# Kernel tuning notes

Hardware: AMD Instinct MI355X
Metric: run time of the kernel (lower is better)

Reference implementation:

```python
import jax, jax.numpy as jnp
import numpy as np
from math import comb

N_DERIV = 4          # num_derivatives
ODE_DIM = 512        # ode_dimension
K = ODE_DIM * (N_DERIV + 1)


def _build_system(n, d):
    # system_matrices_1d: A_1d = flip(pascal), Q_1d = flip(hilbert), chol(Q_1d)
    x = np.arange(n + 1)
    B = np.array([[comb(i, j) for j in range(n + 1)] for i in range(n + 1)], dtype=np.float64)
    A1 = B[::-1, ::-1]                                  # flip both axes
    Hil = 1.0 / (x[:, None] + x[None, :] + 1.0)
    Q1 = Hil[::-1, ::-1]
    L1 = np.linalg.cholesky(Q1)
    a = np.kron(np.eye(d), A1)
    q = np.kron(np.eye(d), L1)
    return jnp.asarray(a, jnp.float32), jnp.asarray(q, jnp.float32)


def _qr_r(x):
    # sqrtm_to_cholesky: upper-triangular factor from reduced QR
    return jnp.linalg.qr(x)[1]


def setup_inputs() -> dict:
    key = jax.random.key(0)
    k1, k2, k3, k4, k5 = jax.random.split(key, 5)
    a, q_sqrtm_lower = _build_system(N_DERIV, ODE_DIM)
    m0 = jax.random.normal(k1, (K,), dtype=jnp.float32)
    l0 = jnp.tril(jax.random.normal(k2, (K, K), dtype=jnp.float32) * 0.05)
    H = jax.random.normal(k3, (ODE_DIM, K), dtype=jnp.float32) * 0.1
    bias = jax.random.normal(k4, (ODE_DIM,), dtype=jnp.float32)
    dt = jax.random.uniform(k5, (1,), dtype=jnp.float32, minval=0.05, maxval=0.15)
    return {"m0": m0, "l0": l0, "H": H, "bias": bias, "dt": dt,
            "a": a, "q_sqrtm_lower": q_sqrtm_lower}


def reference(m0, l0, H, bias, dt, a, q_sqrtm_lower):
    d = H.shape[0]
    k = m0.shape[0]
    n1 = k // d                       # num_derivatives + 1
    # --- assemble_preconditioner ---
    powers = jnp.arange(n1 - 1, -1, -1, dtype=m0.dtype)
    scales = jnp.exp(jax.lax.lgamma(powers + 1.0))
    pw = powers + 0.5
    adt = jnp.abs(dt[0])
    p = jnp.tile(adt ** pw / scales, d)          # (k,)
    p_inv = jnp.tile(adt ** (-pw) * scales, d)   # (k,)
    # --- extrapolate_mean ---
    m0_p = p_inv * m0
    m_ext_p = a @ m0_p
    m_ext = p * m_ext_p
    # EK-style linearized observation residual
    m_obs = H @ m_ext - bias                     # (d,)
    # --- estimate_error ---
    l_obs_ns_e = H @ (p_inv[:, None] * q_sqrtm_lower)            # (d,k)
    l_obs_raw = _qr_r(l_obs_ns_e.T).T                            # lower (d,d)
    res_white = jax.scipy.linalg.solve_triangular(l_obs_raw.T, m_obs, lower=False)
    diffusion = jnp.sqrt(jnp.dot(res_white, res_white) / res_white.size)
    error = diffusion * jnp.sqrt(jnp.einsum('nj,nj->n', l_obs_raw, l_obs_raw))
    # --- complete_extrapolation (sum_of_sqrtm_factors) ---
    R1 = (a @ (p_inv[:, None] * l0)).T           # (k,k)
    R2 = (diffusion * q_sqrtm_lower).T           # (k,k)
    l_ext_p = _qr_r(jnp.vstack([R1, R2])).T      # lower (k,k)
    l_ext = p[:, None] * l_ext_p
    # --- final_correction ---
    l_obs_ns = H @ l_ext                         # (d,k)
    l_obs = _qr_r(l_obs_ns.T).T                  # lower (d,d)
    crosscov = l_ext @ l_obs_ns.T                # (k,d)
    gain = jax.scipy.linalg.cho_solve((l_obs, True), crosscov.T).T  # (k,d)
    m_cor = m_ext - gain @ m_obs
    l_cor = l_ext - gain @ l_obs_ns
    u = jnp.reshape(m_cor, (-1, d), order='F')[0]  # derivative-0 block
    return m_cor, l_cor, u, error, diffusion
```

## Files before the change

kernel.cpp:

```cpp
#include <hip/hip_runtime.h>
#include <math.h>

#define KDIM 2560
#define DDIM 512
#define NB 64

#define QM 2560
#define QM2 1024
#define QN 512
#define PW 16
#define QACT 528

#define OUT_LCOR 2560
#define OUT_U    6556160
#define OUT_ERR  6556672
#define OUT_DIFF 6557184


__global__ void k_setup(const float* dt, double* scal){
  if (threadIdx.x==0 && blockIdx.x==0){
    double adt = fabs((double)dt[0]);
    const double scales[5] = {24.0,6.0,2.0,1.0,1.0};
    for (int i=0;i<5;i++){
      double pw = (double)(4-i)+0.5;
      scal[i]   = pow(adt, pw)/scales[i];
      scal[5+i] = pow(adt,-pw)*scales[i];
    }
  }
}

__global__ __launch_bounds__(256) void k_mext_mobs(const float* a, const float* m0, const float* H,
                                                   const float* bias, const double* scal,
                                                   double* mext, double* mobs){
  __shared__ double me[KDIM];
  __shared__ double red[256];
  double pp[5], pv[5];
  #pragma unroll
  for (int i=0;i<5;i++){ pp[i]=scal[i]; pv[i]=scal[5+i]; }
  int tid=threadIdx.x;
  for (int r=tid; r<KDIM; r+=256){
    int j=r/5, i=r%5;
    const float* arow = a + (size_t)r*KDIM + 5*j;
    const float* m0b  = m0 + 5*j;
    double acc=0;
    #pragma unroll
    for (int l=0;l<5;l++) acc += (double)arow[l]*pv[l]*(double)m0b[l];
    me[r] = pp[i]*acc;
  }
  __syncthreads();
  if (blockIdx.x==0) for (int r=tid;r<KDIM;r+=256) mext[r]=me[r];
  int b = blockIdx.x;
  const float* Hr = H + (size_t)b*KDIM;
  double acc=0;
  for (int c=tid;c<KDIM;c+=256) acc += (double)Hr[c]*me[c];
  red[tid]=acc; __syncthreads();
  for (int s=128;s>0;s>>=1){ if (tid<s) red[tid]+=red[tid+s]; __syncthreads(); }
  if (tid==0) mobs[b] = red[0] - (double)bias[b];
}

__global__ void k_A2(const float* H, const float* q, const double* scal,
                     double* Atop, double* Abot){
  int idx = blockIdx.x*blockDim.x+threadIdx.x;
  if (idx >= QN*QM) return;
  double pv[5];
  #pragma unroll
  for (int t=0;t<5;t++) pv[t]=scal[5+t];
  int j = idx / QM;
  int i = idx % QM;
  int bi = i/5;
  double acc=0;
  #pragma unroll
  for (int t=0;t<5;t++)
    acc += (double)H[(size_t)j*QM + 5*bi+t]*pv[t]*(double)q[(size_t)(5*bi+t)*QM + i];
  if (i < 512) Atop[(size_t)j*QM2 + i] = acc;
  else         Abot[(size_t)j*2048 + (i-512)] = acc;
}

__global__ void k_copyB(const double* Gbot, double* AQ){
  int idx = blockIdx.x*blockDim.x+threadIdx.x;
  if (idx >= 512*512) return;
  int c = idx/512, rr = idx%512;
  AQ[(size_t)c*QM2 + 512 + rr] = (rr<=c) ? Gbot[(size_t)c*512 + rr] : 0.0;
}

__global__ __launch_bounds__(576) void qr_step(double* A, double* vhead, double* Tbufs, int p){
  int col0 = p*PW;
  int tid=threadIdx.x, wid=tid>>6, lane=tid&63;

  if (blockIdx.x > 0){
    int pc0 = col0 - PW;
    const double* T = Tbufs + (size_t)(p-1)*PW*PW;
    int cc = col0 + PW + ((int)blockIdx.x - 1);
    int m = QM2 - pc0; if (m>QACT) m=QACT;
    __shared__ double redu[9][PW];
    __shared__ double yshu[PW];
    __shared__ double wshu[PW];
    int lr = tid;
    double a = (lr<m)? A[(size_t)cc*QM2 + pc0 + lr] : 0.0;
    double vv[PW];
    #pragma unroll
    for (int j=0;j<PW;j++){
      double vj=0.0;
      if (lr<m){
        if (lr>j)       vj=A[(size_t)(pc0+j)*QM2 + pc0 + lr];
        else if (lr==j) vj=vhead[pc0+j];
      }
      vv[j]=vj;
    }
    #pragma unroll
    for (int j=0;j<PW;j++){
      double d=vv[j]*a;
      #pragma unroll
      for (int o=32;o>0;o>>=1) d+=__shfl_down(d,o);
      if (lane==0) redu[wid][j]=d;
    }
    __syncthreads();
    if (tid<PW){
      double y=0;
      #pragma unroll
      for (int t=0;t<9;t++) y+=redu[t][tid];
      yshu[tid]=y;
    }
    __syncthreads();
    if (tid<PW){
      double s=0;
      for (int t=0;t<=tid;t++) s+=T[t*PW+tid]*yshu[t];
      wshu[tid]=s;
    }
    __syncthreads();
    if (lr<m){
      double s=0;
      #pragma unroll
      for (int j=0;j<PW;j++) s+=vv[j]*wshu[j];
      A[(size_t)cc*QM2 + pc0 + lr]=a-s;
    }
    return;
  }

  __shared__ double redw[9][PW];
  __shared__ double rednorm[9];
  __shared__ double sh[3];
  __shared__ double wsh[PW];
  __shared__ double alphas[PW], betas[PW];
  __shared__ double VtVs[PW][PW];
  __shared__ double Tsh[PW][PW];
  __shared__ double redP[9][PW*PW];
  __shared__ double ysh2[PW][PW];
  __shared__ double wsh2[PW][PW];

  int m = QM2 - col0; if (m>QACT) m=QACT;
  bool on = tid < m;
  double x[PW];

  if (p>0){
    int pc0 = col0 - PW;
    const double* T = Tbufs + (size_t)(p-1)*PW*PW;
    int mp = QM2 - pc0; if (mp>QACT) mp=QACT;
    bool gA = on;
    bool gB = (tid>=560);
    int rowA = col0 + tid;
    int kB   = tid - 560;
    double vv[PW];
    #pragma unroll
    for (int j=0;j<PW;j++){
      double vj=0.0;
      if (gA){
        if (tid + PW < mp) vj = A[(size_t)(pc0+j)*QM2 + rowA];
      } else if (gB){
        if (kB>j)       vj=A[(size_t)(pc0+j)*QM2 + pc0 + kB];
        else if (kB==j) vj=vhead[pc0+j];
      }
      vv[j]=vj;
    }
    #pragma unroll
    for (int c=0;c<PW;c++){
      double a=0.0;
      if (gA)      a = A[(size_t)(col0+c)*QM2 + rowA];
      else if (gB) a = A[(size_t)(col0+c)*QM2 + pc0 + kB];
      x[c]=a;
    }
    #pragma unroll
    for (int c=0;c<PW;c++){
      #pragma unroll
      for (int j=0;j<PW;j++){
        double d=vv[j]*x[c];
        #pragma unroll
        for (int o=32;o>0;o>>=1) d+=__shfl_down(d,o);
        if (lane==0) redP[wid][c*PW+j]=d;
      }
    }
    __syncthreads();
    if (tid<PW*PW){
      double y=0;
      #pragma unroll
      for (int t=0;t<9;t++) y+=redP[t][tid];
      ysh2[tid>>4][tid&15]=y;
    }
    __syncthreads();
    if (tid<PW*PW){
      int c=tid>>4, jj=tid&15;
      double s=0;
      for (int t=0;t<=jj;t++) s+=T[t*PW+jj]*ysh2[c][t];
      wsh2[c][jj]=s;
    }
    __syncthreads();
    #pragma unroll
    for (int c=0;c<PW;c++){
      double s=0;
      #pragma unroll
      for (int j=0;j<PW;j++) s+=vv[j]*wsh2[c][j];
      x[c]-=s;
    }
    if (gB){
      #pragma unroll
      for (int c=0;c<PW;c++) A[(size_t)(col0+c)*QM2 + pc0 + kB] = x[c];
    }
    if (!on){
      #pragma unroll
      for (int c=0;c<PW;c++) x[c]=0.0;
    }
    __syncthreads();
  } else {
    #pragma unroll
    for (int j=0;j<PW;j++)
      x[j] = on ? A[(size_t)(col0+j)*QM2 + col0 + tid] : 0.0;
  }

  #pragma unroll
  for (int j=0;j<PW;j++){
    double v0 = (tid>=j && on)? x[j] : 0.0;
    double ps = v0*v0;
    #pragma unroll
    for (int o=32;o>0;o>>=1) ps += __shfl_down(ps,o);
    if (lane==0) rednorm[wid]=ps;
    if (tid==j) sh[0]=x[j];
    __syncthreads();
    if (tid==0){
      double s0=0;
      for (int t=0;t<9;t++) s0+=rednorm[t];
      double x1=sh[0];
      double nrm=sqrt(s0);
      double alpha=(x1>=0.0)?-nrm:nrm;
      double v1=x1-alpha;
      double vtv=s0-2.0*alpha*x1+alpha*alpha;
      double b=(vtv>0.0)?2.0/vtv:0.0;
      sh[1]=v1; sh[2]=b;
      alphas[j]=alpha; betas[j]=b;
      vhead[col0+j]=v1;
    }
    __syncthreads();
    if (tid==j) x[j]=sh[1];
    double b=sh[2];
    double v=(tid>=j && on)? x[j] : 0.0;
    #pragma unroll
    for (int t=0;t<PW;t++){
      if (t==j) continue;
      double pdot=v*x[t];
      #pragma unroll
      for (int o=32;o>0;o>>=1) pdot+=__shfl_down(pdot,o);
      if (lane==0) redw[wid][t]=pdot;
    }
    __syncthreads();
    if (tid<PW && tid!=j){
      double tot=0;
      #pragma unroll
      for (int t2=0;t2<9;t2++) tot+=redw[t2][tid];
      if (tid>j) wsh[tid]=b*tot;
      else       VtVs[tid][j]=tot;
    }
    __syncthreads();
    if (v!=0.0){
      #pragma unroll
      for (int t=j+1;t<PW;t++) x[t]-=wsh[t]*v;
    }
  }
  __syncthreads();
  if (tid<PW){
    int i=tid;
    Tsh[i][i]=betas[i];
    for (int j2=i+1;j2<PW;j2++){
      double z=0;
      for (int t=i;t<j2;t++) z+=Tsh[i][t]*VtVs[t][j2];
      Tsh[i][j2]=-betas[j2]*z;
    }
  }
  __syncthreads();
  for (int e=tid;e<PW*PW;e+=576){
    int i=e/PW, j2=e%PW;
    Tbufs[(size_t)p*PW*PW + e] = (j2>=i)? Tsh[i][j2] : 0.0;
  }
  if (on){
    #pragma unroll
    for (int j=0;j<PW;j++)
      A[(size_t)(col0+j)*QM2 + col0 + tid] = (tid==j)? alphas[j] : x[j];
  }
}

__global__ __launch_bounds__(512) void k_rpost(const double* Aq, const double* mobs,
                                               double* scal, float* out){
  __shared__ double b[DDIM];
  __shared__ double xs[DDIM];
  __shared__ double D[NB][NB+1];
  __shared__ double red[DDIM];
  __shared__ double g1sh[DDIM];
  int tid=threadIdx.x;
  {
    double s=0;
    for (int r=0;r<=tid;r++){ double v=Aq[(size_t)tid*QM2 + r]; s+=v*v; }
    g1sh[tid]=s;
  }
  b[tid]=mobs[tid];
  __syncthreads();
  for (int p=7;p>=0;p--){
    int b0=p*NB;
    for (int e=tid;e<NB*NB;e+=512){ int i=e&63, j2=e>>6; D[i][j2]=Aq[(size_t)(b0+j2)*QM2 + b0+i]; }
    __syncthreads();
    if (tid<64){
      double bi=b[b0+tid];
      for (int k=NB-1;k>=0;k--){
        double bk=__shfl(bi,k);
        double xk=bk/D[k][k];
        if (tid<k) bi-=D[tid][k]*xk;
        if (tid==k) bi=xk;
      }
      xs[b0+tid]=bi;
    }
    __syncthreads();
    if (tid<b0){
      double s=0;
      #pragma unroll 8
      for (int j2=0;j2<NB;j2++) s+=Aq[(size_t)(b0+j2)*QM2 + tid]*xs[b0+j2];
      b[tid]-=s;
    }
    __syncthreads();
  }
  red[tid]=xs[tid]*xs[tid]; __syncthreads();
  for (int s=256;s>0;s>>=1){ if (tid<s) red[tid]+=red[tid+s]; __syncthreads(); }
  double diff=sqrt(red[0]/(double)DDIM);
  if (tid==0){ scal[10]=diff; out[OUT_DIFF]=(float)diff; }
  out[OUT_ERR+tid]=(float)(diff*sqrt(fmax(g1sh[tid],0.0)));
}

__global__ void k_X(const float* a, const float* l0, const double* scal, float* X){
  int idx=blockIdx.x*blockDim.x+threadIdx.x;
  if (idx>=KDIM*KDIM) return;
  double pv[5];
  #pragma unroll
  for (int t=0;t<5;t++) pv[t]=scal[5+t];
  int r=idx/KDIM, c=idx%KDIM;
  int j=r/5;
  const float* arow = a + (size_t)r*KDIM + 5*j;
  double acc=0;
  #pragma unroll
  for (int l=0;l<5;l++)
    acc += (double)arow[l]*pv[l]*(double)l0[(size_t)(5*j+l)*KDIM+c];
  X[idx]=(float)acc;
}

template<typename TA,int ATR,typename TB,int BTR,int MODE>
__global__ __launch_bounds__(256) void gemm32(const TA* __restrict__ A,int lda,
                                              const TB* __restrict__ B,int ldb,
                                              void* __restrict__ Cv,int ldc,
                                              int K,int kmode){
  __shared__ double As[32][33];
  __shared__ double Bs[32][33];
  int tid=threadIdx.x, tx=tid&15, ty=tid>>4;
  int n0=blockIdx.x*32, m0=blockIdx.y*32;
  int ks=0, ke=K;
  if (kmode==1) ks=n0;
  else if (kmode==2) ke=min(K,n0+32);
  else if (kmode==3) ke=min(K,m0+32);
  else if (kmode==4) ks=m0;
  double acc[2][2]={};
  for (int k0=ks;k0<ke;k0+=32){
    if (ATR){
      for (int e=tid;e<32*32;e+=256){int k=e>>5,mm=e&31; As[k][mm]=(double)A[(size_t)(k0+k)*lda+m0+mm];}
    } else {
      for (int e=tid;e<32*32;e+=256){int mm=e>>5,k=e&31; As[k][mm]=(double)A[(size_t)(m0+mm)*lda+k0+k];}
    }
    if (BTR){
      for (int e=tid;e<32*32;e+=256){int nn=e>>5,k=e&31; Bs[k][nn]=(double)B[(size_t)(n0+nn)*ldb+k0+k];}
    } else {
      for (int e=tid;e<32*32;e+=256){int k=e>>5,nn=e&31; Bs[k][nn]=(double)B[(size_t)(k0+k)*ldb+n0+nn];}
    }
    __syncthreads();
    #pragma unroll
    for (int t=0;t<32;t++){
      double av[2],bv[2];
      #pragma unroll
      for (int i=0;i<2;i++){av[i]=As[t][ty+16*i];bv[i]=Bs[t][tx+16*i];}
      #pragma unroll
      for (int i=0;i<2;i++)
        #pragma unroll
        for (int j=0;j<2;j++) acc[i][j]+=av[i]*bv[j];
    }
    __syncthreads();
  }
  #pragma unroll
  for (int i=0;i<2;i++){
    #pragma unroll
    for (int j=0;j<2;j++){
      size_t idx=(size_t)(m0+ty+16*i)*ldc+n0+tx+16*j;
      if (MODE==0) ((double*)Cv)[idx]=acc[i][j];
      else if (MODE==1) ((double*)Cv)[idx]-=acc[i][j];
      else ((float*)Cv)[idx]=(float)acc[i][j];
    }
  }
}

__global__ __launch_bounds__(256) void syrk_lower(const float* __restrict__ X, const float* __restrict__ q,
                                                  const double* __restrict__ scal,
                                                  double* __restrict__ G, int n){
  int t = blockIdx.x;
  int u = (int)((sqrtf(8.0f*(float)t+1.0f)+1.0f)*0.5f);
  while ((u*(u-1))/2 > t) u--;
  while ((u*(u+1))/2 <= t) u++;
  int s = (KDIM/64) - u;
  int r = s + (t - (u*(u-1))/2);
  int S0=s*64, R0=r*64;
  __shared__ double As[16][65];
  __shared__ double Bs[16][65];
  int tid=threadIdx.x, tx=tid&15, ty=tid>>4;
  int kend=min(n, S0+80);
  double acc[4][4]={};
  int mm=tid>>2, f=tid&3;
  for (int k0=0;k0<kend;k0+=16){
    {
      float4 xa = *(const float4*)(X + (size_t)(R0+mm)*n + k0 + 4*f);
      float4 xb = *(const float4*)(X + (size_t)(S0+mm)*n + k0 + 4*f);
      As[4*f+0][mm]=(double)xa.x; As[4*f+1][mm]=(double)xa.y;
      As[4*f+2][mm]=(double)xa.z; As[4*f+3][mm]=(double)xa.w;
      Bs[4*f+0][mm]=(double)xb.x; Bs[4*f+1][mm]=(double)xb.y;
      Bs[4*f+2][mm]=(double)xb.z; Bs[4*f+3][mm]=(double)xb.w;
    }
    __syncthreads();
    #pragma unroll
    for (int t2=0;t2<16;t2++){
      double av[4],bv[4];
      #pragma unroll
      for (int i=0;i<4;i++){av[i]=As[t2][ty+16*i];bv[i]=Bs[t2][tx+16*i];}
      #pragma unroll
      for (int i=0;i<4;i++)
        #pragma unroll
        for (int j=0;j<4;j++) acc[i][j]+=av[i]*bv[j];
    }
    __syncthreads();
  }
  double dd = scal[10]*scal[10];
  #pragma unroll
  for (int i=0;i<4;i++)
    #pragma unroll
    for (int j=0;j<4;j++){
      int rr=R0+ty+16*i, c=S0+tx+16*j;
      double v=acc[i][j];
      if (c<=rr && (rr/5)==(c/5)){
        double qq=0;
        #pragma unroll
        for (int k=0;k<5;k++) qq += (double)q[(size_t)(rr%5)*KDIM+k]*(double)q[(size_t)(c%5)*KDIM+k];
        v += dd*qq;
      }
      G[(size_t)rr*n+c]=v;
    }
}

__global__ __launch_bounds__(256) void chol_diag(double* A, int n, int k0){
  __shared__ double P[NB][NB+1];
  int tid=threadIdx.x;
  for (int e=tid;e<NB*NB;e+=256){int r=e>>6,c=e&63;P[r][c]=A[(size_t)(k0+r)*n+k0+c];}
  int tx=tid&15, ty=tid>>4;
  __syncthreads();
  for (int j=0;j<NB;j++){
    double pj=P[j][j];
    __syncthreads();
    double rpj=1.0/sqrt(fmax(pj,1e-280));
    if (tid>j && tid<NB) P[tid][j]*=rpj;
    if (tid==j) P[j][j]=sqrt(fmax(pj,1e-280));
    __syncthreads();
    #pragma unroll
    for (int a2=0;a2<4;a2++){
      int r=ty+16*a2;
      double lrj=P[r][j];
      #pragma unroll
      for (int b2=0;b2<4;b2++){
        int c=tx+16*b2;
        if (r>j && c>j && c<=r) P[r][c]-=lrj*P[c][j];
      }
    }
    __syncthreads();
  }
  for (int e=tid;e<NB*NB;e+=256){int r=e>>6,c=e&63;A[(size_t)(k0+r)*n+k0+c]=P[r][c];}
}

__global__ __launch_bounds__(256) void chol_step(double* __restrict__ A, int n, int k0){
  __shared__ double Ls[NB][NB+1];
  __shared__ double rec[NB];
  __shared__ double As[16][65];
  __shared__ double Bs[16][65];
  int ts0=k0+NB;
  int t=blockIdx.x;
  int r=(int)((sqrtf(8.0f*(float)t+1.0f)-1.0f)*0.5f);
  while ((r*(r+1))/2 > t) r--;
  while (((r+1)*(r+2))/2 <= t) r++;
  int s=t-(r*(r+1))/2;
  int R0=ts0+r*NB, S0=ts0+s*NB;
  int tid=threadIdx.x, tx=tid&15, ty=tid>>4;
  for (int e=tid;e<NB*NB;e+=256){int rr=e>>6,c=e&63;Ls[rr][c]=A[(size_t)(k0+rr)*n+k0+c];}
  __syncthreads();
  if (tid<NB) rec[tid]=1.0/Ls[tid][tid];
  __syncthreads();
  double ar[NB];
  bool solver = (tid<64) || (tid<128 && s!=r);
  int srow = (tid<64)? (R0+tid) : (S0+(tid-64));
  if (solver){
    #pragma unroll
    for (int c=0;c<NB;c++) ar[c]=A[(size_t)srow*n + k0 + c];
    #pragma unroll
    for (int j=0;j<NB;j++){
      double sv=ar[j];
      #pragma unroll
      for (int t2=0;t2<j;t2++) sv-=ar[t2]*Ls[j][t2];
      ar[j]=sv*rec[j];
    }
  }
  double acc[4][4]={};
  #pragma unroll
  for (int c4=0;c4<4;c4++){
    __syncthreads();
    if (tid<64){
      #pragma unroll
      for (int k=0;k<16;k++) As[k][tid]=ar[c4*16+k];
      if (s==r){
        #pragma unroll
        for (int k=0;k<16;k++) Bs[k][tid]=ar[c4*16+k];
      }
    } else if (tid<128 && s!=r){
      #pragma unroll
      for (int k=0;k<16;k++) Bs[k][tid-64]=ar[c4*16+k];
    }
    __syncthreads();
    #pragma unroll
    for (int tt=0;tt<16;tt++){
      double av[4],bv[4];
      #pragma unroll
      for (int i=0;i<4;i++){av[i]=As[tt][ty+16*i];bv[i]=Bs[tt][tx+16*i];}
      #pragma unroll
      for (int i=0;i<4;i++)
        #pragma unroll
        for (int j=0;j<4;j++) acc[i][j]+=av[i]*bv[j];
    }
  }
  __syncthreads();
  if (t!=0){
    #pragma unroll
    for (int i=0;i<4;i++)
      #pragma unroll
      for (int j=0;j<4;j++)
        A[(size_t)(R0+ty+16*i)*n+S0+tx+16*j]-=acc[i][j];
    return;
  }
  double (*P)[NB+1] = Ls;
  #pragma unroll
  for (int i=0;i<4;i++)
    #pragma unroll
    for (int j=0;j<4;j++)
      P[ty+16*i][tx+16*j] = A[(size_t)(ts0+ty+16*i)*n+ts0+tx+16*j] - acc[i][j];
  __syncthreads();
  for (int j=0;j<NB;j++){
    double pj=P[j][j];
    __syncthreads();
    double rpj=1.0/sqrt(fmax(pj,1e-280));
    if (tid>j && tid<NB) P[tid][j]*=rpj;
    if (tid==j) P[j][j]=sqrt(fmax(pj,1e-280));
    __syncthreads();
    #pragma unroll
    for (int a2=0;a2<4;a2++){
      int r2=ty+16*a2;
      double lrj=P[r2][j];
      #pragma unroll
      for (int b2=0;b2<4;b2++){
        int c=tx+16*b2;
        if (r2>j && c>j && c<=r2) P[r2][c]-=lrj*P[c][j];
      }
    }
    __syncthreads();
  }
  for (int e=tid;e<NB*NB;e+=256){int r2=e>>6,c=e&63;A[(size_t)(ts0+r2)*n+ts0+c]=P[r2][c];}
}

__global__ __launch_bounds__(256) void chol_sweep(double* A, int n){
  __shared__ double Ls[NB][NB+1];
  __shared__ double St[NB][NB+1];
  __shared__ double rec[NB];
  int k0=blockIdx.y*NB;
  int base=k0+NB+blockIdx.x*256;
  if (base>=n) return;
  int tid=threadIdx.x;
  for (int e=tid;e<NB*NB;e+=256){int r2=e>>6,c=e&63;Ls[r2][c]=A[(size_t)(k0+r2)*n+k0+c];}
  __syncthreads();
  if (tid<NB) rec[tid]=1.0/Ls[tid][tid];
  int myrow=base+tid, mychunk=tid>>6, lrow=tid&63;
  double ar[NB];
  for (int ch=0;ch<4;ch++){
    int r0=base+ch*64;
    for (int e=tid;e<NB*NB;e+=256){
      int r2=e>>6,c=e&63;
      if (r0+r2<n) St[r2][c]=A[(size_t)(r0+r2)*n+k0+c];
    }
    __syncthreads();
    if (mychunk==ch && myrow<n){
      #pragma unroll
      for (int c=0;c<NB;c++) ar[c]=St[lrow][c];
    }
    __syncthreads();
  }
  if (myrow<n){
    #pragma unroll
    for (int j=0;j<NB;j++){
      double s2=ar[j];
      #pragma unroll
      for (int t2=0;t2<j;t2++) s2-=ar[t2]*Ls[j][t2];
      ar[j]=s2*rec[j];
    }
  }
  for (int ch=0;ch<4;ch++){
    int r0=base+ch*64;
    if (mychunk==ch && myrow<n){
      #pragma unroll
      for (int c=0;c<NB;c++) St[lrow][c]=ar[c];
    }
    __syncthreads();
    for (int e=tid;e<NB*NB;e+=256){
      int r2=e>>6,c=e&63;
      if (r0+r2<n) A[(size_t)(r0+r2)*n+k0+c]=St[r2][c];
    }
    __syncthreads();
  }
}

__global__ void k_extract(const double* G2, const double* scal, float* lext){
  int idx=blockIdx.x*blockDim.x+threadIdx.x;
  if (idx>=KDIM*KDIM) return;
  int r=idx/KDIM, c=idx%KDIM;
  double v = (c<=r)? scal[r%5]*G2[idx] : 0.0;
  lext[idx]=(float)v;
}

__global__ __launch_bounds__(256) void trinv_diag(const double* S, double* Linv){
  __shared__ double Ls[NB][NB+1];
  __shared__ double Ti[NB][NB+1];
  int jb=blockIdx.x, tid=threadIdx.x;
  for (int e=tid; e<DDIM*NB; e+=256){
    int r=e/NB, c=e%NB;
    Linv[(size_t)r*DDIM + jb*NB + c]=0.0;
  }
  for (int e=tid;e<NB*NB;e+=256){int r=e>>6,c=e&63; Ls[r][c]=S[(size_t)(jb*NB+r)*DDIM + jb*NB+c];}
  __syncthreads();
  if (tid<NB){
    int c=tid;
    for (int r=c;r<NB;r++){
      double s=(r==c)?1.0:0.0;
      for (int t=c;t<r;t++) s-=Ls[r][t]*Ti[t][c];
      Ti[r][c]=s/Ls[r][r];
    }
    for (int r=0;r<c;r++) Ti[r][c]=0.0;
  }
  __syncthreads();
  for (int e=tid;e<NB*NB;e+=256){int r=e>>6,c=e&63; Linv[(size_t)(jb*NB+r)*DDIM + jb*NB+c]=Ti[r][c];}
}

__global__ __launch_bounds__(256) void trinv_step(const double* S, double* Linv, int d){
  __shared__ double As[16][65];
  __shared__ double Bs[16][65];
  __shared__ double Ps[NB][NB+1];
  int jb=blockIdx.x, ib=jb+d;
  int tid=threadIdx.x, tx=tid&15, ty=tid>>4;
  double acc[4][4]={};
  int kstart=jb*NB, kend=ib*NB;
  for (int k0=kstart;k0<kend;k0+=16){
    for (int e=tid;e<64*16;e+=256){int mm=e>>4,k=e&15; As[k][mm]=S[(size_t)(ib*NB+mm)*DDIM + k0+k];}
    for (int e=tid;e<16*64;e+=256){int k=e>>6,nn=e&63; Bs[k][nn]=Linv[(size_t)(k0+k)*DDIM + jb*NB+nn];}
    __syncthreads();
    #pragma unroll
    for (int t=0;t<16;t++){
      double av[4],bv[4];
      #pragma unroll
      for (int i=0;i<4;i++){av[i]=As[t][ty+16*i];bv[i]=Bs[t][tx+16*i];}
      #pragma unroll
      for (int i=0;i<4;i++)
        #pragma unroll
        for (int j=0;j<4;j++) acc[i][j]+=av[i]*bv[j];
    }
    __syncthreads();
  }
  #pragma unroll
  for (int i=0;i<4;i++)
    #pragma unroll
    for (int j=0;j<4;j++) Ps[ty+16*i][tx+16*j]=acc[i][j];
  double o[4][4]={};
  __syncthreads();
  for (int k0=0;k0<NB;k0+=16){
    for (int e=tid;e<64*16;e+=256){int mm=e>>4,k=e&15; As[k][mm]=Linv[(size_t)(ib*NB+mm)*DDIM + ib*NB+k0+k];}
    __syncthreads();
    #pragma unroll
    for (int t=0;t<16;t++){
      double av[4],bv[4];
      #pragma unroll
      for (int i=0;i<4;i++){av[i]=As[t][ty+16*i];bv[i]=Ps[k0+t][tx+16*i];}
      #pragma unroll
      for (int i=0;i<4;i++)
        #pragma unroll
        for (int j=0;j<4;j++) o[i][j]+=av[i]*bv[j];
    }
    __syncthreads();
  }
  #pragma unroll
  for (int i=0;i<4;i++)
    #pragma unroll
    for (int j=0;j<4;j++)
      Linv[(size_t)(ib*NB+ty+16*i)*DDIM + jb*NB+tx+16*j] = -o[i][j];
}

__global__ void k_mcor(const double* Z, const double* mobs, const double* mext, float* out){
  __shared__ double mo[DDIM];
  for (int s=threadIdx.x;s<DDIM;s+=256) mo[s]=mobs[s];
  __syncthreads();
  int r=blockIdx.x*256+threadIdx.x;
  if (r>=KDIM) return;
  double acc=0;
  for (int s=0;s<DDIM;s++) acc += Z[(size_t)s*KDIM+r]*mo[s];
  double mc = mext[r]-acc;
  out[r]=(float)mc;
  if (r%5==0) out[OUT_U + r/5]=(float)mc;
}

__global__ __launch_bounds__(256) void k_lcor(const double* __restrict__ Z, const float* __restrict__ lobs,
                                              const float* __restrict__ lext, float* __restrict__ out){
  __shared__ double As[16][65];
  __shared__ double Bs[16][65];
  int tid=threadIdx.x, tx=tid&15, ty=tid>>4;
  int n0=blockIdx.x*64, m0=blockIdx.y*64;
  double acc[4][4]={};
  int kk=tid>>4, f=tid&15;
  for (int k0=0;k0<DDIM;k0+=16){
    for (int e=tid;e<16*64;e+=256){int k=e>>6,mm=e&63; As[k][mm]=Z[(size_t)(k0+k)*KDIM+m0+mm];}
    {
      float4 xb = *(const float4*)(lobs + (size_t)(k0+kk)*KDIM + n0 + 4*f);
      Bs[kk][4*f+0]=(double)xb.x; Bs[kk][4*f+1]=(double)xb.y;
      Bs[kk][4*f+2]=(double)xb.z; Bs[kk][4*f+3]=(double)xb.w;
    }
    __syncthreads();
    #pragma unroll
    for (int t=0;t<16;t++){
      double av[4],bv[4];
      #pragma unroll
      for (int i=0;i<4;i++){av[i]=As[t][ty+16*i];bv[i]=Bs[t][tx+16*i];}
      #pragma unroll
      for (int i=0;i<4;i++)
        #pragma unroll
        for (int j=0;j<4;j++) acc[i][j]+=av[i]*bv[j];
    }
    __syncthreads();
  }
  #pragma unroll
  for (int i=0;i<4;i++)
    #pragma unroll
    for (int j=0;j<4;j++){
      size_t idx=(size_t)(m0+ty+16*i)*KDIM+n0+tx+16*j;
      out[OUT_LCOR+idx]=(float)((double)lext[idx]-acc[i][j]);
    }
}

extern "C" void kernel_launch(void* const* d_in, const int* in_sizes, int n_in,
                              void* d_out, int out_size, void* d_ws, size_t ws_size,
                              hipStream_t stream) {
  const float* m0  = (const float*)d_in[0];
  const float* l0  = (const float*)d_in[1];
  const float* H   = (const float*)d_in[2];
  const float* bias= (const float*)d_in[3];
  const float* dt  = (const float*)d_in[4];
  const float* a   = (const float*)d_in[5];
  const float* q   = (const float*)d_in[6];
  float* out = (float*)d_out;

  char* w=(char*)d_ws;
  auto alloc=[&](size_t bytes)->char*{ char* p=w; w += ((bytes+255)/256)*256; return p; };
  double* scal  =(double*)alloc(16*8);
  double* mext  =(double*)alloc((size_t)KDIM*8);
  double* mobs  =(double*)alloc((size_t)DDIM*8);
  double* vheadA=(double*)alloc((size_t)QN*8);
  double* Tbufs =(double*)alloc((size_t)(QN/PW)*PW*PW*8);
  double* AQ    =(double*)alloc((size_t)QM2*QN*8);
  double* S     =(double*)alloc((size_t)DDIM*DDIM*8);
  double* G2    =(double*)alloc((size_t)KDIM*KDIM*8);
  float*  LOBS  =(float*) alloc((size_t)DDIM*KDIM*4);
  float*  X     =(float*) alloc((size_t)KDIM*KDIM*4);
  float*  LEXT  = X;
  double* Abot  = G2;
  double* Gbot  = Abot + (size_t)2048*512;
  double* Linv  = G2;
  double* C2    = Linv + (size_t)DDIM*DDIM;
  double* Y     = C2   + (size_t)DDIM*KDIM;
  double* Z     = Y    + (size_t)DDIM*KDIM;

  auto chol_full=[&](double* M, int n){
    chol_diag<<<1,256,0,stream>>>(M, n, 0);
    for (int k0=0;k0+NB<n;k0+=NB){
      int T = (n-k0-NB)/NB;
      chol_step<<<T*(T+1)/2,256,0,stream>>>(M,n,k0);
    }
    dim3 g((n-NB+255)/256, n/NB-1);
    chol_sweep<<<g,256,0,stream>>>(M,n);
  };

  k_setup<<<1,1,0,stream>>>(dt, scal);
  k_mext_mobs<<<DDIM,256,0,stream>>>(a, m0, H, bias, scal, mext, mobs);

  k_A2<<<(QN*QM+255)/256,256,0,stream>>>(H, q, scal, AQ, Abot);
  gemm32<double,0,double,1,0><<<dim3(16,16),256,0,stream>>>(Abot,2048, Abot,2048, Gbot,512, 2048, 0);
  chol_full(Gbot, 512);
  k_copyB<<<(512*512+255)/256,256,0,stream>>>(Gbot, AQ);
  for (int p=0;p<QN/PW;p++){
    int nlz = QN - (p+1)*PW;
    int grid = 1 + ((p>0)? nlz : 0);
    qr_step<<<grid,576,0,stream>>>(AQ, vheadA, Tbufs, p);
  }
  k_rpost<<<1,512,0,stream>>>(AQ, mobs, scal, out);

  k_X<<<(KDIM*KDIM+255)/256,256,0,stream>>>(a, l0, scal, X);
  syrk_lower<<<(KDIM/64)*((KDIM/64)+1)/2,256,0,stream>>>(X, q, scal, G2, KDIM);
  chol_full(G2, KDIM);
  k_extract<<<(KDIM*KDIM+255)/256,256,0,stream>>>(G2, scal, LEXT);

  gemm32<float,0,float,0,2><<<dim3(KDIM/32,DDIM/32),256,0,stream>>>(H,KDIM, LEXT,KDIM, LOBS,KDIM, KDIM, 1);
  gemm32<float,0,float,1,0><<<dim3(DDIM/32,DDIM/32),256,0,stream>>>(LOBS,KDIM, LOBS,KDIM, S,DDIM, KDIM, 0);
  chol_full(S, DDIM);
  trinv_diag<<<8,256,0,stream>>>(S, Linv);
  for (int d=1;d<8;d++)
    trinv_step<<<8-d,256,0,stream>>>(S, Linv, d);
  gemm32<float,0,float,1,0><<<dim3(KDIM/32,DDIM/32),256,0,stream>>>(LOBS,KDIM, LEXT,KDIM, C2,KDIM, KDIM, 2);
  gemm32<double,0,double,0,0><<<dim3(KDIM/32,DDIM/32),256,0,stream>>>(Linv,DDIM, C2,KDIM, Y,KDIM, DDIM, 3);
  gemm32<double,1,double,0,0><<<dim3(KDIM/32,DDIM/32),256,0,stream>>>(Linv,DDIM, Y,KDIM, Z,KDIM, DDIM, 4);

  k_mcor<<<(KDIM+255)/256,256,0,stream>>>(Z, mobs, mext, out);
  k_lcor<<<dim3(KDIM/64,KDIM/64),256,0,stream>>>(Z, LOBS, LEXT, out);
}
```

Baseline: 15.00 ms.

## Fuse setup and copy kernels, merge triangular-inverse steps, widen SYRK k-tile

Four separate changes. The scale-factor setup kernel is folded into the mean-extrapolation kernel, and the Gbot-to-AQ copy is folded into the first QR step: extra blocks do the copy while block 0 reads Gbot directly. The seven trinv_step launches become one trinv_all launch in which each column block loops over its row blocks in order. The SYRK kernel now stages 32 k-values per shared-memory tile instead of 16, halving its barrier count at the cost of more shared memory per block. These mainly cut kernel launches and synchronisation, but the merged triangular inverse runs the whole dependency chain serially inside single blocks.

Measured after the change: 15.19 ms. No clear change (+1.3%).

```diff
diff --git a/kernel.cpp b/kernel.cpp
--- a/kernel.cpp
+++ b/kernel.cpp
@@ -17,27 +17,27 @@
 #define OUT_DIFF 6557184
 
 
-__global__ void k_setup(const float* dt, double* scal){
-  if (threadIdx.x==0 && blockIdx.x==0){
-    double adt = fabs((double)dt[0]);
-    const double scales[5] = {24.0,6.0,2.0,1.0,1.0};
-    for (int i=0;i<5;i++){
-      double pw = (double)(4-i)+0.5;
-      scal[i]   = pow(adt, pw)/scales[i];
-      scal[5+i] = pow(adt,-pw)*scales[i];
-    }
-  }
-}
-
 __global__ __launch_bounds__(256) void k_mext_mobs(const float* a, const float* m0, const float* H,
-                                                   const float* bias, const double* scal,
-                                                   double* mext, double* mobs){
+                                                   const float* bias, const float* dt,
+                                                   double* scal, double* mext, double* mobs){
   __shared__ double me[KDIM];
   __shared__ double red[256];
   double pp[5], pv[5];
-  #pragma unroll
-  for (int i=0;i<5;i++){ pp[i]=scal[i]; pv[i]=scal[5+i]; }
+  {
+    double adt = fabs((double)dt[0]);
+    const double scales5[5] = {24.0,6.0,2.0,1.0,1.0};
+    #pragma unroll
+    for (int i=0;i<5;i++){
+      double pw = (double)(4-i)+0.5;
+      pp[i]=pow(adt, pw)/scales5[i];
+      pv[i]=pow(adt,-pw)*scales5[i];
+    }
+  }
   int tid=threadIdx.x;
+  if (blockIdx.x==0 && tid==0){
+    #pragma unroll
+    for (int i=0;i<5;i++){ scal[i]=pp[i]; scal[5+i]=pv[i]; }
+  }
   for (int r=tid; r<KDIM; r+=256){
     int j=r/5, i=r%5;
     const float* arow = a + (size_t)r*KDIM + 5*j;
@@ -76,18 +76,20 @@
   else         Abot[(size_t)j*2048 + (i-512)] = acc;
 }
 
-__global__ void k_copyB(const double* Gbot, double* AQ){
-  int idx = blockIdx.x*blockDim.x+threadIdx.x;
-  if (idx >= 512*512) return;
-  int c = idx/512, rr = idx%512;
-  AQ[(size_t)c*QM2 + 512 + rr] = (rr<=c) ? Gbot[(size_t)c*512 + rr] : 0.0;
-}
-
-__global__ __launch_bounds__(576) void qr_step(double* A, double* vhead, double* Tbufs, int p){
+__global__ __launch_bounds__(576) void qr_step(double* A, double* vhead, double* Tbufs,
+                                               const double* Gbot, int p){
   int col0 = p*PW;
   int tid=threadIdx.x, wid=tid>>6, lane=tid&63;
 
   if (blockIdx.x > 0){
+    if (p==0){
+      int idx=((int)blockIdx.x-1)*576+tid;
+      if (idx < 496*512){
+        int c=16+idx/512, rr=idx%512;
+        A[(size_t)c*QM2 + 512 + rr] = (rr<=c)? Gbot[(size_t)c*512+rr] : 0.0;
+      }
+      return;
+    }
     int pc0 = col0 - PW;
     const double* T = Tbufs + (size_t)(p-1)*PW*PW;
     int cc = col0 + PW + ((int)blockIdx.x - 1);
@@ -222,8 +224,15 @@
     __syncthreads();
   } else {
     #pragma unroll
-    for (int j=0;j<PW;j++)
-      x[j] = on ? A[(size_t)(col0+j)*QM2 + col0 + tid] : 0.0;
+    for (int j=0;j<PW;j++){
+      double v=0.0;
+      if (tid<512) v = A[(size_t)j*QM2 + tid];
+      else if (tid<QACT){
+        int rr=tid-512;
+        v = (rr<=j)? Gbot[(size_t)j*512+rr] : 0.0;
+      }
+      x[j]=v;
+    }
   }
 
   #pragma unroll
@@ -418,13 +427,13 @@
   int s = (KDIM/64) - u;
   int r = s + (t - (u*(u-1))/2);
   int S0=s*64, R0=r*64;
-  __shared__ double As[16][65];
-  __shared__ double Bs[16][65];
+  __shared__ double As[32][65];
+  __shared__ double Bs[32][65];
   int tid=threadIdx.x, tx=tid&15, ty=tid>>4;
   int kend=min(n, S0+80);
   double acc[4][4]={};
   int mm=tid>>2, f=tid&3;
-  for (int k0=0;k0<kend;k0+=16){
+  for (int k0=0;k0<kend;k0+=32){
     {
       float4 xa = *(const float4*)(X + (size_t)(R0+mm)*n + k0 + 4*f);
       float4 xb = *(const float4*)(X + (size_t)(S0+mm)*n + k0 + 4*f);
@@ -432,10 +441,21 @@
       As[4*f+2][mm]=(double)xa.z; As[4*f+3][mm]=(double)xa.w;
       Bs[4*f+0][mm]=(double)xb.x; Bs[4*f+1][mm]=(double)xb.y;
       Bs[4*f+2][mm]=(double)xb.z; Bs[4*f+3][mm]=(double)xb.w;
-    }
-    __syncthreads();
-    #pragma unroll
-    for (int t2=0;t2<16;t2++){
+      if (k0+16 < kend){
+        float4 ya = *(const float4*)(X + (size_t)(R0+mm)*n + k0 + 16 + 4*f);
+        float4 yb = *(const float4*)(X + (size_t)(S0+mm)*n + k0 + 16 + 4*f);
+        As[16+4*f+0][mm]=(double)ya.x; As[16+4*f+1][mm]=(double)ya.y;
+        As[16+4*f+2][mm]=(double)ya.z; As[16+4*f+3][mm]=(double)ya.w;
+        Bs[16+4*f+0][mm]=(double)yb.x; Bs[16+4*f+1][mm]=(double)yb.y;
+        Bs[16+4*f+2][mm]=(double)yb.z; Bs[16+4*f+3][mm]=(double)yb.w;
+      } else {
+        #pragma unroll
+        for (int i=0;i<4;i++){ As[16+4*f+i][mm]=0.0; Bs[16+4*f+i][mm]=0.0; }
+      }
+    }
+    __syncthreads();
+    #pragma unroll
+    for (int t2=0;t2<32;t2++){
       double av[4],bv[4];
       #pragma unroll
       for (int i=0;i<4;i++){av[i]=As[t2][ty+16*i];bv[i]=Bs[t2][tx+16*i];}
@@ -668,56 +688,59 @@
   for (int e=tid;e<NB*NB;e+=256){int r=e>>6,c=e&63; Linv[(size_t)(jb*NB+r)*DDIM + jb*NB+c]=Ti[r][c];}
 }
 
-__global__ __launch_bounds__(256) void trinv_step(const double* S, double* Linv, int d){
+__global__ __launch_bounds__(256) void trinv_all(const double* S, double* Linv){
   __shared__ double As[16][65];
   __shared__ double Bs[16][65];
   __shared__ double Ps[NB][NB+1];
-  int jb=blockIdx.x, ib=jb+d;
+  int jb=blockIdx.x;
   int tid=threadIdx.x, tx=tid&15, ty=tid>>4;
-  double acc[4][4]={};
-  int kstart=jb*NB, kend=ib*NB;
-  for (int k0=kstart;k0<kend;k0+=16){
-    for (int e=tid;e<64*16;e+=256){int mm=e>>4,k=e&15; As[k][mm]=S[(size_t)(ib*NB+mm)*DDIM + k0+k];}
-    for (int e=tid;e<16*64;e+=256){int k=e>>6,nn=e&63; Bs[k][nn]=Linv[(size_t)(k0+k)*DDIM + jb*NB+nn];}
-    __syncthreads();
-    #pragma unroll
-    for (int t=0;t<16;t++){
-      double av[4],bv[4];
-      #pragma unroll
-      for (int i=0;i<4;i++){av[i]=As[t][ty+16*i];bv[i]=Bs[t][tx+16*i];}
-      #pragma unroll
-      for (int i=0;i<4;i++)
-        #pragma unroll
-        for (int j=0;j<4;j++) acc[i][j]+=av[i]*bv[j];
-    }
-    __syncthreads();
-  }
-  #pragma unroll
-  for (int i=0;i<4;i++)
-    #pragma unroll
-    for (int j=0;j<4;j++) Ps[ty+16*i][tx+16*j]=acc[i][j];
-  double o[4][4]={};
-  __syncthreads();
-  for (int k0=0;k0<NB;k0+=16){
-    for (int e=tid;e<64*16;e+=256){int mm=e>>4,k=e&15; As[k][mm]=Linv[(size_t)(ib*NB+mm)*DDIM + ib*NB+k0+k];}
-    __syncthreads();
-    #pragma unroll
-    for (int t=0;t<16;t++){
-      double av[4],bv[4];
-      #pragma unroll
-      for (int i=0;i<4;i++){av[i]=As[t][ty+16*i];bv[i]=Ps[k0+t][tx+16*i];}
-      #pragma unroll
-      for (int i=0;i<4;i++)
-        #pragma unroll
-        for (int j=0;j<4;j++) o[i][j]+=av[i]*bv[j];
-    }
-    __syncthreads();
-  }
-  #pragma unroll
-  for (int i=0;i<4;i++)
-    #pragma unroll
-    for (int j=0;j<4;j++)
-      Linv[(size_t)(ib*NB+ty+16*i)*DDIM + jb*NB+tx+16*j] = -o[i][j];
+  for (int ib=jb+1; ib<8; ib++){
+    double acc[4][4]={};
+    int kstart=jb*NB, kend=ib*NB;
+    for (int k0=kstart;k0<kend;k0+=16){
+      for (int e=tid;e<64*16;e+=256){int mm=e>>4,k=e&15; As[k][mm]=S[(size_t)(ib*NB+mm)*DDIM + k0+k];}
+      for (int e=tid;e<16*64;e+=256){int k=e>>6,nn=e&63; Bs[k][nn]=Linv[(size_t)(k0+k)*DDIM + jb*NB+nn];}
+      __syncthreads();
+      #pragma unroll
+      for (int t=0;t<16;t++){
+        double av[4],bv[4];
+        #pragma unroll
+        for (int i=0;i<4;i++){av[i]=As[t][ty+16*i];bv[i]=Bs[t][tx+16*i];}
+        #pragma unroll
+        for (int i=0;i<4;i++)
+          #pragma unroll
+          for (int j=0;j<4;j++) acc[i][j]+=av[i]*bv[j];
+      }
+      __syncthreads();
+    }
+    #pragma unroll
+    for (int i=0;i<4;i++)
+      #pragma unroll
+      for (int j=0;j<4;j++) Ps[ty+16*i][tx+16*j]=acc[i][j];
+    double o[4][4]={};
+    __syncthreads();
+    for (int k0=0;k0<NB;k0+=16){
+      for (int e=tid;e<64*16;e+=256){int mm=e>>4,k=e&15; As[k][mm]=Linv[(size_t)(ib*NB+mm)*DDIM + ib*NB+k0+k];}
+      __syncthreads();
+      #pragma unroll
+      for (int t=0;t<16;t++){
+        double av[4],bv[4];
+        #pragma unroll
+        for (int i=0;i<4;i++){av[i]=As[t][ty+16*i];bv[i]=Ps[k0+t][tx+16*i];}
+        #pragma unroll
+        for (int i=0;i<4;i++)
+          #pragma unroll
+          for (int j=0;j<4;j++) o[i][j]+=av[i]*bv[j];
+      }
+      __syncthreads();
+    }
+    #pragma unroll
+    for (int i=0;i<4;i++)
+      #pragma unroll
+      for (int j=0;j<4;j++)
+        Linv[(size_t)(ib*NB+ty+16*i)*DDIM + jb*NB+tx+16*j] = -o[i][j];
+    __syncthreads();
+  }
 }
 
 __global__ void k_mcor(const double* Z, const double* mobs, const double* mext, float* out){
@@ -812,17 +835,16 @@
     chol_sweep<<<g,256,0,stream>>>(M,n);
   };
 
-  k_setup<<<1,1,0,stream>>>(dt, scal);
-  k_mext_mobs<<<DDIM,256,0,stream>>>(a, m0, H, bias, scal, mext, mobs);
+  k_mext_mobs<<<DDIM,256,0,stream>>>(a, m0, H, bias, dt, scal, mext, mobs);
 
   k_A2<<<(QN*QM+255)/256,256,0,stream>>>(H, q, scal, AQ, Abot);
   gemm32<double,0,double,1,0><<<dim3(16,16),256,0,stream>>>(Abot,2048, Abot,2048, Gbot,512, 2048, 0);
   chol_full(Gbot, 512);
-  k_copyB<<<(512*512+255)/256,256,0,stream>>>(Gbot, AQ);
   for (int p=0;p<QN/PW;p++){
-    int nlz = QN - (p+1)*PW;
-    int grid = 1 + ((p>0)? nlz : 0);
-    qr_step<<<grid,576,0,stream>>>(AQ, vheadA, Tbufs, p);
+    int grid;
+    if (p==0) grid = 1 + (496*512 + 575)/576;
+    else      grid = 1 + (QN - (p+1)*PW);
+    qr_step<<<grid,576,0,stream>>>(AQ, vheadA, Tbufs, Gbot, p);
   }
   k_rpost<<<1,512,0,stream>>>(AQ, mobs, scal, out);
 
@@ -835,8 +857,7 @@
   gemm32<float,0,float,1,0><<<dim3(DDIM/32,DDIM/32),256,0,stream>>>(LOBS,KDIM, LOBS,KDIM, S,DDIM, KDIM, 0);
   chol_full(S, DDIM);
   trinv_diag<<<8,256,0,stream>>>(S, Linv);
-  for (int d=1;d<8;d++)
-    trinv_step<<<8-d,256,0,stream>>>(S, Linv, d);
+  trinv_all<<<8,256,0,stream>>>(S, Linv);
   gemm32<float,0,float,1,0><<<dim3(KDIM/32,DDIM/32),256,0,stream>>>(LOBS,KDIM, LEXT,KDIM, C2,KDIM, KDIM, 2);
   gemm32<double,0,double,0,0><<<dim3(KDIM/32,DDIM/32),256,0,stream>>>(Linv,DDIM, C2,KDIM, Y,KDIM, DDIM, 3);
   gemm32<double,1,double,0,0><<<dim3(KDIM/32,DDIM/32),256,0,stream>>>(Linv,DDIM, Y,KDIM, Z,KDIM, DDIM, 4);
```
